# Kernel tuning notes

Hardware: AMD Instinct MI355X
Metric: run time of the kernel (lower is better)

The kernel has to match this reference:

```python
import jax, jax.numpy as jnp
import numpy as np

N_RADIAL = 8
N_PSEUDO = 4          # Alchemical pseudo-species
EMB_DIM = N_RADIAL * N_PSEUDO  # 32
CUTOFF = 5.0
WIDTH = 0.5
SQRT3_4PI = float(np.sqrt(3.0 / (4.0 * np.pi)))


def _cg_111():
    # Real Clebsch-Gordan coefficients for l1=l2=1 -> L=1.
    # In the real spherical-harmonic ordering (-1,0,1) = (y,z,x) this is the
    # Levi-Civita tensor (permuted), scaled by 1/sqrt(2).
    eps = np.zeros((3, 3, 3), dtype=np.float32)
    for i, j, k in [(0, 1, 2), (1, 2, 0), (2, 0, 1)]:
        eps[i, j, k] = 1.0
        eps[i, k, j] = -1.0
    perm = np.array([1, 2, 0])  # (m=-1,0,1) -> cartesian (y,z,x)
    C = eps[np.ix_(perm, perm, perm)] / np.sqrt(2.0)
    return jnp.asarray(C, dtype=jnp.float32)


def _shifted_cosine(r):
    # ShiftedCosine cutoff function: 1 below rc-w, smooth cosine in [rc-w, rc], 0 above.
    t = (r - (CUTOFF - WIDTH)) / WIDTH
    f = 0.5 * (1.0 + jnp.cos(jnp.pi * jnp.clip(t, 0.0, 1.0)))
    return jnp.where(r < CUTOFF, f, 0.0)


def _radial_basis(r):
    # Laplacian-eigenstate-like radial functions: spherical-Bessel-type sin modes.
    # r: (E,) -> (E, N_RADIAL)
    n = jnp.arange(1, N_RADIAL + 1, dtype=jnp.float32)  # (N_RADIAL,)
    arg = (jnp.pi / CUTOFF) * r[:, None] * n[None, :]
    return jnp.sin(arg) / (r[:, None] + 1e-10)


def setup_inputs() -> dict:
    key = jax.random.key(0)
    k1, k2, k3, k4, k5, k6, k7 = jax.random.split(key, 7)
    E, A, T = 2_000_000, 50_000, 4
    # edge vectors within the cutoff sphere (scaled so |v| mostly < CUTOFF)
    vecs = jax.random.normal(k1, (E, 3), dtype=jnp.float32) * 1.8
    centers = jax.random.randint(k2, (E,), 0, A, dtype=jnp.int32)
    neighbors = jax.random.randint(k3, (E,), 0, A, dtype=jnp.int32)
    species = jax.random.randint(k4, (A,), 0, T, dtype=jnp.int32)
    # learned parameters
    W_species = jax.random.normal(k5, (T, N_PSEUDO), dtype=jnp.float32) * 0.5  # alchemical neighbor embedding
    Emb = jax.random.normal(k6, (T, EMB_DIM), dtype=jnp.float32) * 0.5         # center encoding
    Wc = jax.random.normal(k7, (EMB_DIM, 3), dtype=jnp.float32) * 0.2          # contraction to 3 basis vectors
    return {"interatomic_vectors": vecs, "W_species": W_species, "Emb": Emb,
            "Wc": Wc, "centers": centers, "neighbors": neighbors, "species": species}


def reference(interatomic_vectors, W_species, Emb, Wc, centers, neighbors, species):
    A = species.shape[0]
    E = interatomic_vectors.shape[0]
    r = jnp.linalg.norm(interatomic_vectors, axis=-1)            # (E,)
    fcut = _shifted_cosine(r)                                    # (E,)
    R = _radial_basis(r) * fcut[:, None]                         # (E, n)
    # l=1 real spherical harmonics, (m=-1,0,1) = (y,z,x)/r
    Y = SQRT3_4PI * interatomic_vectors[:, (1, 2, 0)] / (r[:, None] + 1e-10)  # (E, 3)
    edge_feat = Y[:, :, None] * R[:, None, :]                    # (E, 3, n)
    # alchemical neighbor weights
    pseudo = W_species[species[neighbors]]                       # (E, q)
    full = jnp.einsum('emn,eq->emnq', edge_feat, pseudo).reshape(E, 3, EMB_DIM)
    # neighbor-sum spherical expansion per center atom
    spex = jax.ops.segment_sum(full, centers, num_segments=A)   # (A, 3, d)
    # center-type encoding
    spex = spex * Emb[species][:, None, :]                       # (A, 3, d)
    # contract radial/chemical channels to 3 basis vectors
    v = jnp.einsum('amd,dk->amk', spex, Wc)                      # (A, 3mu, 3basis)
    C = _cg_111()
    v3 = jnp.einsum('im,in,mnp->ip', v[:, :, 0], v[:, :, 1], C)  # (A, 3)
    basis = jnp.stack([v[:, :, 0], v[:, :, 1], v3], axis=2)      # (A, 3, 3)
    return basis
```

## Files before the change

kernel.cpp:

```cpp
#include <hip/hip_runtime.h>
#include <hip/hip_fp16.h>
#include <math.h>

#define N_RADIAL 8
#define N_PSEUDO 4
#define EMB_DIM 32
#define CUTOFF 5.0f
#define WIDTH 0.5f
#define SQRT3_4PI 0.48860251190291992f
#define INV_SQRT2 0.70710678118654752f
#define PI_F 3.14159265358979323846f

#define SLICE_SHIFT 8
#define SLICE_SZ 256
#define MAX_NSLICE 1024
#define SCAT_EPB 8192
#define SCAT_THREADS 1024
#define SCAT_GROUPS 2
#define ACC_THREADS 1024
#define MAX_SPEC_WORDS 4096

#define Q_INV 8192.0f
#define Q 1.220703125e-4
#define BIAS_ENC 131072.0f
#define ENC_MAX 262143.0f
#define FIELD_MASK 0x3FFFFFFULL

__global__ void init_kernel(const float* __restrict__ W_species,
                            const float* __restrict__ Emb,
                            const float* __restrict__ Wc,
                            const int*   __restrict__ species,
                            float* __restrict__ G,
                            unsigned int* __restrict__ cursor,
                            unsigned int* __restrict__ spec_packed,
                            int A, int nslice, int cap, int words) {
    int tid = blockIdx.x * blockDim.x + threadIdx.x;

    if (blockIdx.x == 0) {
        int i = threadIdx.x;
        if (i < 256) {
            int k  = i & 1;
            int n  = (i >> 1) & 7;
            int tn = (i >> 4) & 3;
            int tc = i >> 6;
            float acc = 0.0f;
            #pragma unroll
            for (int q = 0; q < N_PSEUDO; ++q) {
                int d = n * N_PSEUDO + q;
                acc += W_species[tn * N_PSEUDO + q] * Emb[tc * EMB_DIM + d] * Wc[d * 3 + k];
            }
            G[i] = acc;
        }
        for (int s = i; s < nslice; s += (int)blockDim.x)
            cursor[s] = (unsigned int)(s * cap);
    }

    for (int w = tid; w < words; w += (int)(gridDim.x * blockDim.x)) {
        unsigned int v = 0;
        int base = w * 16;
        #pragma unroll
        for (int j = 0; j < 16; ++j) {
            int a = base + j;
            if (a < A) v |= ((unsigned int)species[a] & 3u) << (2 * j);
        }
        spec_packed[w] = v;
    }
}

__device__ __forceinline__ bool edge_products(float vx, float vy, float vz,
                                              const float* __restrict__ Gp,
                                              float pr[6]) {
    float r = sqrtf(vx * vx + vy * vy + vz * vz);
    if (r >= CUTOFF) return false;

    float rinv = 1.0f / (r + 1e-10f);

    float t = fminf(fmaxf((r - (CUTOFF - WIDTH)) * (1.0f / WIDTH), 0.0f), 1.0f);
    float fcut = 0.5f * (1.0f + __cosf(PI_F * t));

    float theta = (PI_F / CUTOFF) * r;
    float s1 = __sinf(theta);
    float c1 = __cosf(theta);
    float twoc  = 2.0f * c1;
    float sn_m1 = 0.0f;
    float sn    = s1;

    float s0 = 0.0f, s1a = 0.0f;
    #pragma unroll
    for (int n = 0; n < N_RADIAL; ++n) {
        s0  = fmaf(sn, Gp[n * 2 + 0], s0);
        s1a = fmaf(sn, Gp[n * 2 + 1], s1a);
        float nxt = twoc * sn - sn_m1;
        sn_m1 = sn;
        sn = nxt;
    }
    float coef = rinv * fcut;
    s0 *= coef; s1a *= coef;

    float Y0 = SQRT3_4PI * vy * rinv;
    float Y1 = SQRT3_4PI * vz * rinv;
    float Y2 = SQRT3_4PI * vx * rinv;

    pr[0] = Y0 * s0; pr[1] = Y0 * s1a;
    pr[2] = Y1 * s0; pr[3] = Y1 * s1a;
    pr[4] = Y2 * s0; pr[5] = Y2 * s1a;
    return true;
}

__device__ __forceinline__ void encode_edge(float vx, float vy, float vz,
                                            int c, int nb,
                                            const unsigned int* __restrict__ spec,
                                            unsigned long long& word, int& sl) {
    float r2 = vx * vx + vy * vy + vz * vz;
    if (r2 < CUTOFF * CUTOFF) {
        unsigned int tc = (spec[c >> 4]  >> ((c & 15) << 1)) & 3u;
        unsigned int tn = (spec[nb >> 4] >> ((nb & 15) << 1)) & 3u;
        unsigned int meta = (unsigned int)(c & (SLICE_SZ - 1)) | (tc << 8) | (tn << 10);
        unsigned int hx = (unsigned int)__half_as_ushort(__float2half(vx));
        unsigned int hy = (unsigned int)__half_as_ushort(__float2half(vy));
        unsigned int hz = (unsigned int)__half_as_ushort(__float2half(vz));
        word = ((unsigned long long)(hz | (meta << 16)) << 32)
             | (unsigned long long)(hx | (hy << 16));
        sl = c >> SLICE_SHIFT;
    }
}

__global__ __launch_bounds__(SCAT_THREADS)
void scatter_kernel(const float* __restrict__ vecs,
                    const int*   __restrict__ centers,
                    const int*   __restrict__ neighbors,
                    const unsigned int* __restrict__ spec_packed,
                    unsigned int* __restrict__ cursor,
                    unsigned long long* __restrict__ payload,
                    int E, int nslice, int cap, int words) {
    __shared__ unsigned int hist[MAX_NSLICE];
    __shared__ unsigned int spec[MAX_SPEC_WORDS];

    for (int i = threadIdx.x; i < nslice; i += blockDim.x) hist[i] = 0u;
    for (int i = threadIdx.x; i < words; i += blockDim.x) spec[i] = spec_packed[i];
    __syncthreads();

    const int beg = blockIdx.x * SCAT_EPB;

    unsigned long long word[SCAT_GROUPS * 4];
    int sl[SCAT_GROUPS * 4];

    #pragma unroll
    for (int g = 0; g < SCAT_GROUPS; ++g) {
        int e0 = beg + g * (SCAT_THREADS * 4) + (int)threadIdx.x * 4;
        #pragma unroll
        for (int j = 0; j < 4; ++j) { sl[g * 4 + j] = -1; word[g * 4 + j] = 0; }

        if (e0 + 4 <= E) {
            const float4* vp = (const float4*)vecs + ((e0 * 3) >> 2);
            float4 v0 = vp[0], v1 = vp[1], v2 = vp[2];
            int4 c4 = ((const int4*)centers)[e0 >> 2];
            int4 n4 = ((const int4*)neighbors)[e0 >> 2];

            encode_edge(v0.x, v0.y, v0.z, c4.x, n4.x, spec, word[g*4+0], sl[g*4+0]);
            encode_edge(v0.w, v1.x, v1.y, c4.y, n4.y, spec, word[g*4+1], sl[g*4+1]);
            encode_edge(v1.z, v1.w, v2.x, c4.z, n4.z, spec, word[g*4+2], sl[g*4+2]);
            encode_edge(v2.y, v2.z, v2.w, c4.w, n4.w, spec, word[g*4+3], sl[g*4+3]);
        } else {
            #pragma unroll
            for (int j = 0; j < 4; ++j) {
                int e = e0 + j;
                if (e < E) {
                    encode_edge(vecs[3*e], vecs[3*e+1], vecs[3*e+2],
                                centers[e], neighbors[e], spec,
                                word[g*4+j], sl[g*4+j]);
                }
            }
        }

        #pragma unroll
        for (int j = 0; j < 4; ++j)
            if (sl[g * 4 + j] >= 0) atomicAdd(&hist[sl[g * 4 + j]], 1u);
    }
    __syncthreads();

    for (int s = threadIdx.x; s < nslice; s += (int)blockDim.x) {
        unsigned int c = hist[s];
        hist[s] = c ? atomicAdd(&cursor[s], c) : 0u;
    }
    __syncthreads();

    #pragma unroll
    for (int k = 0; k < SCAT_GROUPS * 4; ++k) {
        if (sl[k] >= 0) {
            unsigned int pos = atomicAdd(&hist[sl[k]], 1u);
            if (pos < (unsigned int)((sl[k] + 1) * cap))
                payload[pos] = word[k];
        }
    }
}

__global__ __launch_bounds__(ACC_THREADS)
void accum_kernel(const unsigned long long* __restrict__ payload,
                  const unsigned int* __restrict__ cursor,
                  const float* __restrict__ G,
                  float* __restrict__ out, int A, int cap) {
    __shared__ float Gs[256];
    __shared__ unsigned long long acc64[SLICE_SZ * 3];
    int s = blockIdx.x;

    if (threadIdx.x < 256) Gs[threadIdx.x] = G[threadIdx.x];
    for (int i = threadIdx.x; i < SLICE_SZ * 3; i += blockDim.x) acc64[i] = 0ull;
    __syncthreads();

    unsigned int beg = (unsigned int)(s * cap);
    unsigned int end = min(cursor[s], (unsigned int)((s + 1) * cap));
    for (unsigned int i = beg + threadIdx.x; i < end; i += blockDim.x) {
        unsigned long long w = payload[i];
        unsigned int lo = (unsigned int)w;
        unsigned int hi = (unsigned int)(w >> 32);
        float vx = __half2float(__ushort_as_half((unsigned short)(lo & 0xffffu)));
        float vy = __half2float(__ushort_as_half((unsigned short)(lo >> 16)));
        float vz = __half2float(__ushort_as_half((unsigned short)(hi & 0xffffu)));
        unsigned int meta = hi >> 16;
        int lid = (int)(meta & (SLICE_SZ - 1));
        int tc  = (int)((meta >> 8) & 3);
        int tn  = (int)((meta >> 10) & 3);
        const float* Gp = &Gs[((tc * 4 + tn) * 8) * 2];

        float pr[6];
        if (!edge_products(vx, vy, vz, Gp, pr)) continue;

        unsigned long long* ap = &acc64[lid * 3];
        #pragma unroll
        for (int j = 0; j < 3; ++j) {
            float el = fminf(fmaxf(fmaf(pr[2 * j + 0], Q_INV, BIAS_ENC) + 0.5f, 0.0f), ENC_MAX);
            float eh = fminf(fmaxf(fmaf(pr[2 * j + 1], Q_INV, BIAS_ENC) + 0.5f, 0.0f), ENC_MAX);
            unsigned long long wrd = (1ULL << 52)
                                   | ((unsigned long long)(unsigned int)eh << 26)
                                   | (unsigned long long)(unsigned int)el;
            atomicAdd(ap + j, wrd);
        }
    }
    __syncthreads();

    for (int lid = threadIdx.x; lid < SLICE_SZ; lid += (int)blockDim.x) {
        int a = s * SLICE_SZ + lid;
        if (a >= A) break;
        const unsigned long long* wv = &acc64[lid * 3];
        float v[6];
        #pragma unroll
        for (int j = 0; j < 3; ++j) {
            unsigned long long x = wv[j];
            float n = (float)(unsigned int)(x >> 52);
            v[2 * j + 0] = (float)((double)(x & FIELD_MASK)         * Q) - n * 16.0f;
            v[2 * j + 1] = (float)((double)((x >> 26) & FIELD_MASK) * Q) - n * 16.0f;
        }

        float a0 = v[0], b0 = v[1];
        float a1 = v[2], b1 = v[3];
        float a2 = v[4], b2 = v[5];

        float c0 = (a1 * b2 - a2 * b1) * INV_SQRT2;
        float c1 = (a2 * b0 - a0 * b2) * INV_SQRT2;
        float c2 = (a0 * b1 - a1 * b0) * INV_SQRT2;

        float* o = out + (size_t)a * 9;
        o[0] = a0; o[1] = b0; o[2] = c0;
        o[3] = a1; o[4] = b1; o[5] = c1;
        o[6] = a2; o[7] = b2; o[8] = c2;
    }
}

__global__ void edge_kernel_fb(const float* __restrict__ vecs,
                               const int* __restrict__ centers,
                               const int* __restrict__ neighbors,
                               const int* __restrict__ species,
                               const float* __restrict__ G,
                               unsigned long long* __restrict__ vacc, int E) {
    __shared__ float Gs[256];
    Gs[threadIdx.x] = G[threadIdx.x];
    __syncthreads();

    int e = blockIdx.x * blockDim.x + threadIdx.x;
    if (e >= E) return;

    float vx = vecs[3 * e + 0], vy = vecs[3 * e + 1], vz = vecs[3 * e + 2];
    int c = centers[e];
    int tc = species[c];
    int tn = species[neighbors[e]];
    const float* Gp = &Gs[((tc * 4 + tn) * 8) * 2];

    float pr[6];
    if (!edge_products(vx, vy, vz, Gp, pr)) return;

    unsigned long long* base = vacc + (size_t)c * 4;
    #pragma unroll
    for (int j = 0; j < 3; ++j) {
        float el = fminf(fmaxf(fmaf(pr[2 * j + 0], Q_INV, BIAS_ENC) + 0.5f, 0.0f), ENC_MAX);
        float eh = fminf(fmaxf(fmaf(pr[2 * j + 1], Q_INV, BIAS_ENC) + 0.5f, 0.0f), ENC_MAX);
        unsigned long long w = (1ULL << 52)
                             | ((unsigned long long)(unsigned int)eh << 26)
                             | (unsigned long long)(unsigned int)el;
        atomicAdd(base + j, w);
    }
}

__global__ void finalize_fb(const unsigned long long* __restrict__ vacc,
                            float* __restrict__ out, int A) {
    int a = blockIdx.x * blockDim.x + threadIdx.x;
    if (a >= A) return;

    const unsigned long long* w = vacc + (size_t)a * 4;
    double v[6];
    #pragma unroll
    for (int j = 0; j < 3; ++j) {
        unsigned long long x = w[j];
        double n = (double)(x >> 52);
        v[2 * j + 0] = (double)(x & FIELD_MASK)         * (double)Q - n * 16.0;
        v[2 * j + 1] = (double)((x >> 26) & FIELD_MASK) * (double)Q - n * 16.0;
    }
    float a0 = (float)v[0], b0 = (float)v[1];
    float a1 = (float)v[2], b1 = (float)v[3];
    float a2 = (float)v[4], b2 = (float)v[5];
    float c0 = (a1 * b2 - a2 * b1) * INV_SQRT2;
    float c1 = (a2 * b0 - a0 * b2) * INV_SQRT2;
    float c2 = (a0 * b1 - a1 * b0) * INV_SQRT2;
    float* o = out + (size_t)a * 9;
    o[0] = a0; o[1] = b0; o[2] = c0;
    o[3] = a1; o[4] = b1; o[5] = c1;
    o[6] = a2; o[7] = b2; o[8] = c2;
}

extern "C" void kernel_launch(void* const* d_in, const int* in_sizes, int n_in,
                              void* d_out, int out_size, void* d_ws, size_t ws_size,
                              hipStream_t stream) {
    const float* vecs      = (const float*)d_in[0];
    const float* W_species = (const float*)d_in[1];
    const float* Emb       = (const float*)d_in[2];
    const float* Wc        = (const float*)d_in[3];
    const int*   centers   = (const int*)d_in[4];
    const int*   neighbors = (const int*)d_in[5];
    const int*   species   = (const int*)d_in[6];

    int E = in_sizes[0] / 3;
    int A = in_sizes[6];

    int nslice = (A + SLICE_SZ - 1) / SLICE_SZ;
    int words  = (A + 15) / 16;

    double mean = (double)E / (double)nslice;
    int cap = (int)((mean + 8.0 * sqrt(mean) + 63.0) / 64.0) * 64;

    size_t payloadBytes = (size_t)nslice * (size_t)cap * 8;
    size_t metaBytes    = ((size_t)nslice + 256 + (size_t)words) * 4 + 256;
    bool sort_path = (nslice <= MAX_NSLICE) && (words <= MAX_SPEC_WORDS) &&
                     (ws_size >= payloadBytes + metaBytes);

    if (sort_path) {
        unsigned long long* payload = (unsigned long long*)d_ws;
        unsigned int* cursor = (unsigned int*)((char*)d_ws + payloadBytes);
        float*        G      = (float*)(cursor + nslice);
        unsigned int* spec_packed = (unsigned int*)(G + 256);

        int nbi = max(1, (words + 1023) / 1024);
        init_kernel<<<nbi, 1024, 0, stream>>>(W_species, Emb, Wc, species,
                                              G, cursor, spec_packed,
                                              A, nslice, cap, words);
        int nbs = (E + SCAT_EPB - 1) / SCAT_EPB;
        scatter_kernel<<<nbs, SCAT_THREADS, 0, stream>>>(
            vecs, centers, neighbors, spec_packed, cursor, payload,
            E, nslice, cap, words);
        accum_kernel<<<nslice, ACC_THREADS, 0, stream>>>(
            payload, cursor, G, (float*)d_out, A, cap);
    } else {
        unsigned long long* vacc = (unsigned long long*)d_ws;
        float* G = (float*)(vacc + (size_t)A * 4);
        unsigned int* cursor_dummy = (unsigned int*)(G + 256);
        (void)hipMemsetAsync(vacc, 0, (size_t)A * 4 * sizeof(unsigned long long), stream);
        init_kernel<<<1, 1024, 0, stream>>>(W_species, Emb, Wc, species,
                                            G, cursor_dummy, cursor_dummy,
                                            0, 0, 0, 0);
        const int threads = 256;
        edge_kernel_fb<<<(E + threads - 1) / threads, threads, 0, stream>>>(
            vecs, centers, neighbors, species, G, vacc, E);
        finalize_fb<<<(A + threads - 1) / threads, threads, 0, stream>>>(
            vacc, (float*)d_out, A);
    }
}
```

Baseline: 48.14 us.

## Stage scattered edges in shared memory sorted by slice for contiguous payload writes

The scatter kernel now counting-sorts each block's encoded edges by slice in LDS. It uses a wave-level prefix scan over the slice histogram, then writes them to the global payload in a contiguous sweep, where each thread finds its slice by binary search. This replaces scattered 8-byte global stores with mostly coalesced runs per slice. Block size halves to 512 threads and 4096 edges, and the packed species table is read from global memory instead of being copied into LDS. The sort path is now limited to 256 slices, which the 50k-atom input still satisfies. In exchange it adds extra LDS traffic, more barriers and the binary search.

```diff
diff --git a/kernel.cpp b/kernel.cpp
--- a/kernel.cpp
+++ b/kernel.cpp
@@ -13,10 +13,10 @@
 
 #define SLICE_SHIFT 8
 #define SLICE_SZ 256
-#define MAX_NSLICE 1024
-#define SCAT_EPB 8192
-#define SCAT_THREADS 1024
-#define SCAT_GROUPS 2
+#define MAXS 256
+#define SCAT_EPB 4096
+#define SCAT_THREADS 512
+#define SCAT_ITER 8
 #define ACC_THREADS 1024
 #define MAX_SPEC_WORDS 4096
 
@@ -132,21 +132,23 @@
                     const unsigned int* __restrict__ spec_packed,
                     unsigned int* __restrict__ cursor,
                     unsigned long long* __restrict__ payload,
-                    int E, int nslice, int cap, int words) {
-    __shared__ unsigned int hist[MAX_NSLICE];
-    __shared__ unsigned int spec[MAX_SPEC_WORDS];
+                    int E, int nslice, int cap) {
+    __shared__ unsigned long long stage[SCAT_EPB];
+    __shared__ unsigned int hist[MAXS];
+    __shared__ unsigned int lcnt[MAXS];
+    __shared__ unsigned int gbase[MAXS];
+    __shared__ unsigned int lstart[MAXS + 1];
 
     for (int i = threadIdx.x; i < nslice; i += blockDim.x) hist[i] = 0u;
-    for (int i = threadIdx.x; i < words; i += blockDim.x) spec[i] = spec_packed[i];
     __syncthreads();
 
     const int beg = blockIdx.x * SCAT_EPB;
 
-    unsigned long long word[SCAT_GROUPS * 4];
-    int sl[SCAT_GROUPS * 4];
+    unsigned long long word[SCAT_ITER];
+    int sl[SCAT_ITER];
 
     #pragma unroll
-    for (int g = 0; g < SCAT_GROUPS; ++g) {
+    for (int g = 0; g < SCAT_ITER / 4; ++g) {
         int e0 = beg + g * (SCAT_THREADS * 4) + (int)threadIdx.x * 4;
         #pragma unroll
         for (int j = 0; j < 4; ++j) { sl[g * 4 + j] = -1; word[g * 4 + j] = 0; }
@@ -157,17 +159,17 @@
             int4 c4 = ((const int4*)centers)[e0 >> 2];
             int4 n4 = ((const int4*)neighbors)[e0 >> 2];
 
-            encode_edge(v0.x, v0.y, v0.z, c4.x, n4.x, spec, word[g*4+0], sl[g*4+0]);
-            encode_edge(v0.w, v1.x, v1.y, c4.y, n4.y, spec, word[g*4+1], sl[g*4+1]);
-            encode_edge(v1.z, v1.w, v2.x, c4.z, n4.z, spec, word[g*4+2], sl[g*4+2]);
-            encode_edge(v2.y, v2.z, v2.w, c4.w, n4.w, spec, word[g*4+3], sl[g*4+3]);
+            encode_edge(v0.x, v0.y, v0.z, c4.x, n4.x, spec_packed, word[g*4+0], sl[g*4+0]);
+            encode_edge(v0.w, v1.x, v1.y, c4.y, n4.y, spec_packed, word[g*4+1], sl[g*4+1]);
+            encode_edge(v1.z, v1.w, v2.x, c4.z, n4.z, spec_packed, word[g*4+2], sl[g*4+2]);
+            encode_edge(v2.y, v2.z, v2.w, c4.w, n4.w, spec_packed, word[g*4+3], sl[g*4+3]);
         } else {
             #pragma unroll
             for (int j = 0; j < 4; ++j) {
                 int e = e0 + j;
                 if (e < E) {
                     encode_edge(vecs[3*e], vecs[3*e+1], vecs[3*e+2],
-                                centers[e], neighbors[e], spec,
+                                centers[e], neighbors[e], spec_packed,
                                 word[g*4+j], sl[g*4+j]);
                 }
             }
@@ -179,19 +181,51 @@
     }
     __syncthreads();
 
+    if (threadIdx.x < 64) {
+        int lane  = (int)threadIdx.x;
+        int chunk = (nslice + 63) / 64;
+        int lo = lane * chunk;
+        int hi = min(lo + chunk, nslice);
+
+        unsigned int sum = 0;
+        for (int i = lo; i < hi; ++i) sum += hist[i];
+
+        unsigned int inc = sum;
+        #pragma unroll
+        for (int d = 1; d < 64; d <<= 1) {
+            unsigned int o = __shfl_up(inc, d, 64);
+            if (lane >= d) inc += o;
+        }
+        unsigned int run = inc - sum;
+        for (int i = lo; i < hi; ++i) { lstart[i] = run; run += hist[i]; }
+        if (lane == 63) lstart[nslice] = run;
+    }
     for (int s = threadIdx.x; s < nslice; s += (int)blockDim.x) {
         unsigned int c = hist[s];
-        hist[s] = c ? atomicAdd(&cursor[s], c) : 0u;
+        gbase[s] = c ? atomicAdd(&cursor[s], c) : 0u;
+        lcnt[s]  = 0u;
     }
     __syncthreads();
 
     #pragma unroll
-    for (int k = 0; k < SCAT_GROUPS * 4; ++k) {
+    for (int k = 0; k < SCAT_ITER; ++k) {
         if (sl[k] >= 0) {
-            unsigned int pos = atomicAdd(&hist[sl[k]], 1u);
-            if (pos < (unsigned int)((sl[k] + 1) * cap))
-                payload[pos] = word[k];
-        }
+            unsigned int loff = atomicAdd(&lcnt[sl[k]], 1u);
+            stage[lstart[sl[k]] + loff] = word[k];
+        }
+    }
+    __syncthreads();
+
+    unsigned int total = lstart[nslice];
+    for (unsigned int idx = threadIdx.x; idx < total; idx += blockDim.x) {
+        int lo = 0, hi = nslice;
+        while (hi - lo > 1) {
+            int mid = (lo + hi) >> 1;
+            if (lstart[mid] <= idx) lo = mid; else hi = mid;
+        }
+        unsigned int dest = gbase[lo] + (idx - lstart[lo]);
+        if (dest < (unsigned int)((lo + 1) * cap))
+            payload[dest] = stage[idx];
     }
 }
 
@@ -349,7 +383,7 @@
 
     size_t payloadBytes = (size_t)nslice * (size_t)cap * 8;
     size_t metaBytes    = ((size_t)nslice + 256 + (size_t)words) * 4 + 256;
-    bool sort_path = (nslice <= MAX_NSLICE) && (words <= MAX_SPEC_WORDS) &&
+    bool sort_path = (nslice <= MAXS) && (words <= MAX_SPEC_WORDS) &&
                      (ws_size >= payloadBytes + metaBytes);
 
     if (sort_path) {
@@ -365,7 +399,7 @@
         int nbs = (E + SCAT_EPB - 1) / SCAT_EPB;
         scatter_kernel<<<nbs, SCAT_THREADS, 0, stream>>>(
             vecs, centers, neighbors, spec_packed, cursor, payload,
-            E, nslice, cap, words);
+            E, nslice, cap);
         accum_kernel<<<nslice, ACC_THREADS, 0, stream>>>(
             payload, cursor, G, (float*)d_out, A, cap);
     } else {
```

Measured after the change: 52.63 us. 9.3% more time.

## Drop init kernel: build G per block, memset counts, read species directly

Applied to the files above, without the earlier changes.

Removes the separate init kernel. Each accumulate block now builds the 256-entry G table in LDS itself, slice counters are zeroed with a memset, and payload slots are indexed as slice*cap plus a relative offset. The scatter kernel now reads species straight from global memory instead of a 2-bit packed LDS copy. This cuts a launch and the LDS staging of packed species, at the cost of random global gathers on species, more LDS atomics on a smaller histogram, and a lower slice limit (256) for taking the sort path.

```diff
diff --git a/kernel.cpp b/kernel.cpp
--- a/kernel.cpp
+++ b/kernel.cpp
@@ -13,12 +13,11 @@
 
 #define SLICE_SHIFT 8
 #define SLICE_SZ 256
-#define MAX_NSLICE 1024
+#define MAXS 256
 #define SCAT_EPB 8192
 #define SCAT_THREADS 1024
 #define SCAT_GROUPS 2
 #define ACC_THREADS 1024
-#define MAX_SPEC_WORDS 4096
 
 #define Q_INV 8192.0f
 #define Q 1.220703125e-4
@@ -26,44 +25,23 @@
 #define ENC_MAX 262143.0f
 #define FIELD_MASK 0x3FFFFFFULL
 
-__global__ void init_kernel(const float* __restrict__ W_species,
-                            const float* __restrict__ Emb,
-                            const float* __restrict__ Wc,
-                            const int*   __restrict__ species,
-                            float* __restrict__ G,
-                            unsigned int* __restrict__ cursor,
-                            unsigned int* __restrict__ spec_packed,
-                            int A, int nslice, int cap, int words) {
-    int tid = blockIdx.x * blockDim.x + threadIdx.x;
-
-    if (blockIdx.x == 0) {
-        int i = threadIdx.x;
-        if (i < 256) {
-            int k  = i & 1;
-            int n  = (i >> 1) & 7;
-            int tn = (i >> 4) & 3;
-            int tc = i >> 6;
-            float acc = 0.0f;
-            #pragma unroll
-            for (int q = 0; q < N_PSEUDO; ++q) {
-                int d = n * N_PSEUDO + q;
-                acc += W_species[tn * N_PSEUDO + q] * Emb[tc * EMB_DIM + d] * Wc[d * 3 + k];
-            }
-            G[i] = acc;
-        }
-        for (int s = i; s < nslice; s += (int)blockDim.x)
-            cursor[s] = (unsigned int)(s * cap);
-    }
-
-    for (int w = tid; w < words; w += (int)(gridDim.x * blockDim.x)) {
-        unsigned int v = 0;
-        int base = w * 16;
-        #pragma unroll
-        for (int j = 0; j < 16; ++j) {
-            int a = base + j;
-            if (a < A) v |= ((unsigned int)species[a] & 3u) << (2 * j);
-        }
-        spec_packed[w] = v;
+__device__ __forceinline__ void build_G_lds(const float* __restrict__ W_species,
+                                            const float* __restrict__ Emb,
+                                            const float* __restrict__ Wc,
+                                            float* __restrict__ Gs) {
+    if (threadIdx.x < 256) {
+        int i  = threadIdx.x;
+        int k  = i & 1;
+        int n  = (i >> 1) & 7;
+        int tn = (i >> 4) & 3;
+        int tc = i >> 6;
+        float acc = 0.0f;
+        #pragma unroll
+        for (int q = 0; q < N_PSEUDO; ++q) {
+            int d = n * N_PSEUDO + q;
+            acc += W_species[tn * N_PSEUDO + q] * Emb[tc * EMB_DIM + d] * Wc[d * 3 + k];
+        }
+        Gs[i] = acc;
     }
 }
 
@@ -109,12 +87,12 @@
 
 __device__ __forceinline__ void encode_edge(float vx, float vy, float vz,
                                             int c, int nb,
-                                            const unsigned int* __restrict__ spec,
+                                            const int* __restrict__ species,
                                             unsigned long long& word, int& sl) {
     float r2 = vx * vx + vy * vy + vz * vz;
     if (r2 < CUTOFF * CUTOFF) {
-        unsigned int tc = (spec[c >> 4]  >> ((c & 15) << 1)) & 3u;
-        unsigned int tn = (spec[nb >> 4] >> ((nb & 15) << 1)) & 3u;
+        unsigned int tc = (unsigned int)species[c] & 3u;
+        unsigned int tn = (unsigned int)species[nb] & 3u;
         unsigned int meta = (unsigned int)(c & (SLICE_SZ - 1)) | (tc << 8) | (tn << 10);
         unsigned int hx = (unsigned int)__half_as_ushort(__float2half(vx));
         unsigned int hy = (unsigned int)__half_as_ushort(__float2half(vy));
@@ -129,15 +107,13 @@
 void scatter_kernel(const float* __restrict__ vecs,
                     const int*   __restrict__ centers,
                     const int*   __restrict__ neighbors,
-                    const unsigned int* __restrict__ spec_packed,
-                    unsigned int* __restrict__ cursor,
+                    const int*   __restrict__ species,
+                    unsigned int* __restrict__ count,
                     unsigned long long* __restrict__ payload,
-                    int E, int nslice, int cap, int words) {
-    __shared__ unsigned int hist[MAX_NSLICE];
-    __shared__ unsigned int spec[MAX_SPEC_WORDS];
+                    int E, int nslice, int cap) {
+    __shared__ unsigned int hist[MAXS];
 
     for (int i = threadIdx.x; i < nslice; i += blockDim.x) hist[i] = 0u;
-    for (int i = threadIdx.x; i < words; i += blockDim.x) spec[i] = spec_packed[i];
     __syncthreads();
 
     const int beg = blockIdx.x * SCAT_EPB;
@@ -157,17 +133,17 @@
             int4 c4 = ((const int4*)centers)[e0 >> 2];
             int4 n4 = ((const int4*)neighbors)[e0 >> 2];
 
-            encode_edge(v0.x, v0.y, v0.z, c4.x, n4.x, spec, word[g*4+0], sl[g*4+0]);
-            encode_edge(v0.w, v1.x, v1.y, c4.y, n4.y, spec, word[g*4+1], sl[g*4+1]);
-            encode_edge(v1.z, v1.w, v2.x, c4.z, n4.z, spec, word[g*4+2], sl[g*4+2]);
-            encode_edge(v2.y, v2.z, v2.w, c4.w, n4.w, spec, word[g*4+3], sl[g*4+3]);
+            encode_edge(v0.x, v0.y, v0.z, c4.x, n4.x, species, word[g*4+0], sl[g*4+0]);
+            encode_edge(v0.w, v1.x, v1.y, c4.y, n4.y, species, word[g*4+1], sl[g*4+1]);
+            encode_edge(v1.z, v1.w, v2.x, c4.z, n4.z, species, word[g*4+2], sl[g*4+2]);
+            encode_edge(v2.y, v2.z, v2.w, c4.w, n4.w, species, word[g*4+3], sl[g*4+3]);
         } else {
             #pragma unroll
             for (int j = 0; j < 4; ++j) {
                 int e = e0 + j;
                 if (e < E) {
                     encode_edge(vecs[3*e], vecs[3*e+1], vecs[3*e+2],
-                                centers[e], neighbors[e], spec,
+                                centers[e], neighbors[e], species,
                                 word[g*4+j], sl[g*4+j]);
                 }
             }
@@ -181,37 +157,39 @@
 
     for (int s = threadIdx.x; s < nslice; s += (int)blockDim.x) {
         unsigned int c = hist[s];
-        hist[s] = c ? atomicAdd(&cursor[s], c) : 0u;
+        hist[s] = c ? atomicAdd(&count[s], c) : 0u;
     }
     __syncthreads();
 
     #pragma unroll
     for (int k = 0; k < SCAT_GROUPS * 4; ++k) {
         if (sl[k] >= 0) {
-            unsigned int pos = atomicAdd(&hist[sl[k]], 1u);
-            if (pos < (unsigned int)((sl[k] + 1) * cap))
-                payload[pos] = word[k];
+            unsigned int rel = atomicAdd(&hist[sl[k]], 1u);
+            if (rel < (unsigned int)cap)
+                payload[(size_t)sl[k] * cap + rel] = word[k];
         }
     }
 }
 
 __global__ __launch_bounds__(ACC_THREADS)
 void accum_kernel(const unsigned long long* __restrict__ payload,
-                  const unsigned int* __restrict__ cursor,
-                  const float* __restrict__ G,
+                  const unsigned int* __restrict__ count,
+                  const float* __restrict__ W_species,
+                  const float* __restrict__ Emb,
+                  const float* __restrict__ Wc,
                   float* __restrict__ out, int A, int cap) {
     __shared__ float Gs[256];
     __shared__ unsigned long long acc64[SLICE_SZ * 3];
     int s = blockIdx.x;
 
-    if (threadIdx.x < 256) Gs[threadIdx.x] = G[threadIdx.x];
+    build_G_lds(W_species, Emb, Wc, Gs);
     for (int i = threadIdx.x; i < SLICE_SZ * 3; i += blockDim.x) acc64[i] = 0ull;
     __syncthreads();
 
-    unsigned int beg = (unsigned int)(s * cap);
-    unsigned int end = min(cursor[s], (unsigned int)((s + 1) * cap));
-    for (unsigned int i = beg + threadIdx.x; i < end; i += blockDim.x) {
-        unsigned long long w = payload[i];
+    unsigned int cnt = min(count[s], (unsigned int)cap);
+    size_t base = (size_t)s * cap;
+    for (unsigned int i = threadIdx.x; i < cnt; i += blockDim.x) {
+        unsigned long long w = payload[base + i];
         unsigned int lo = (unsigned int)w;
         unsigned int hi = (unsigned int)(w >> 32);
         float vx = __half2float(__ushort_as_half((unsigned short)(lo & 0xffffu)));
@@ -267,14 +245,17 @@
     }
 }
 
-__global__ void edge_kernel_fb(const float* __restrict__ vecs,
-                               const int* __restrict__ centers,
-                               const int* __restrict__ neighbors,
-                               const int* __restrict__ species,
-                               const float* __restrict__ G,
-                               unsigned long long* __restrict__ vacc, int E) {
+__global__ __launch_bounds__(256)
+void edge_kernel_fb(const float* __restrict__ vecs,
+                    const int* __restrict__ centers,
+                    const int* __restrict__ neighbors,
+                    const int* __restrict__ species,
+                    const float* __restrict__ W_species,
+                    const float* __restrict__ Emb,
+                    const float* __restrict__ Wc,
+                    unsigned long long* __restrict__ vacc, int E) {
     __shared__ float Gs[256];
-    Gs[threadIdx.x] = G[threadIdx.x];
+    build_G_lds(W_species, Emb, Wc, Gs);
     __syncthreads();
 
     int e = blockIdx.x * blockDim.x + threadIdx.x;
@@ -342,43 +323,30 @@
     int A = in_sizes[6];
 
     int nslice = (A + SLICE_SZ - 1) / SLICE_SZ;
-    int words  = (A + 15) / 16;
 
     double mean = (double)E / (double)nslice;
     int cap = (int)((mean + 8.0 * sqrt(mean) + 63.0) / 64.0) * 64;
 
     size_t payloadBytes = (size_t)nslice * (size_t)cap * 8;
-    size_t metaBytes    = ((size_t)nslice + 256 + (size_t)words) * 4 + 256;
-    bool sort_path = (nslice <= MAX_NSLICE) && (words <= MAX_SPEC_WORDS) &&
-                     (ws_size >= payloadBytes + metaBytes);
+    size_t metaBytes    = (size_t)nslice * 4 + 256;
+    bool sort_path = (nslice <= MAXS) && (ws_size >= payloadBytes + metaBytes);
 
     if (sort_path) {
         unsigned long long* payload = (unsigned long long*)d_ws;
-        unsigned int* cursor = (unsigned int*)((char*)d_ws + payloadBytes);
-        float*        G      = (float*)(cursor + nslice);
-        unsigned int* spec_packed = (unsigned int*)(G + 256);
-
-        int nbi = max(1, (words + 1023) / 1024);
-        init_kernel<<<nbi, 1024, 0, stream>>>(W_species, Emb, Wc, species,
-                                              G, cursor, spec_packed,
-                                              A, nslice, cap, words);
+        unsigned int* count = (unsigned int*)((char*)d_ws + payloadBytes);
+
+        (void)hipMemsetAsync(count, 0, (size_t)nslice * sizeof(unsigned int), stream);
         int nbs = (E + SCAT_EPB - 1) / SCAT_EPB;
         scatter_kernel<<<nbs, SCAT_THREADS, 0, stream>>>(
-            vecs, centers, neighbors, spec_packed, cursor, payload,
-            E, nslice, cap, words);
+            vecs, centers, neighbors, species, count, payload, E, nslice, cap);
         accum_kernel<<<nslice, ACC_THREADS, 0, stream>>>(
-            payload, cursor, G, (float*)d_out, A, cap);
+            payload, count, W_species, Emb, Wc, (float*)d_out, A, cap);
     } else {
         unsigned long long* vacc = (unsigned long long*)d_ws;
-        float* G = (float*)(vacc + (size_t)A * 4);
-        unsigned int* cursor_dummy = (unsigned int*)(G + 256);
         (void)hipMemsetAsync(vacc, 0, (size_t)A * 4 * sizeof(unsigned long long), stream);
-        init_kernel<<<1, 1024, 0, stream>>>(W_species, Emb, Wc, species,
-                                            G, cursor_dummy, cursor_dummy,
-                                            0, 0, 0, 0);
         const int threads = 256;
         edge_kernel_fb<<<(E + threads - 1) / threads, threads, 0, stream>>>(
-            vecs, centers, neighbors, species, G, vacc, E);
+            vecs, centers, neighbors, species, W_species, Emb, Wc, vacc, E);
         finalize_fb<<<(A + threads - 1) / threads, threads, 0, stream>>>(
             vacc, (float*)d_out, A);
     }
```

After: 53.29 us. 1.11x slower.
